# Kernel tuning notes

Hardware: AMD Instinct MI355X
Metric: run time of the kernel (lower is better)

Reference implementation:

```python
import jax, jax.numpy as jnp
import numpy as np

N_STEPS = 2
MAX_STEP = 1.0
EPS64 = float(np.finfo(np.float64).eps)


def _sphere_log(p, q):
    # log map on unit sphere, tangent at p pointing to q; p,q: [..., D]
    cos = jnp.clip(jnp.sum(p * q, axis=-1, keepdims=True), -1.0, 1.0)
    u = q - cos * p
    un = jnp.linalg.norm(u, axis=-1, keepdims=True)
    theta = jnp.arccos(cos)
    return theta * u / (un + 1e-12)


def _sphere_exp(p, v):
    # exp map on unit sphere; jnp.sinc(n/pi) = sin(n)/n (stable at 0)
    n = jnp.linalg.norm(v, axis=-1, keepdims=True)
    x = jnp.cos(n) * p + jnp.sinc(n / jnp.pi) * v
    return x / jnp.linalg.norm(x, axis=-1, keepdims=True)


def setup_inputs() -> dict:
    key = jax.random.key(0)
    ks = jax.random.split(key, 6)
    N, C, D, E = 50000, 16, 3, 1600000
    nodes = jax.random.normal(ks[0], (N, C, D), dtype=jnp.float32)
    nodes = nodes / jnp.linalg.norm(nodes, axis=-1, keepdims=True)  # points on S^2
    edge_w = jax.random.uniform(ks[1], (E,), dtype=jnp.float32)
    senders = jax.random.randint(ks[2], (E,), 0, N, dtype=jnp.int32)
    receivers = jax.random.randint(ks[3], (E,), 0, N, dtype=jnp.int32)
    t_sqrt = 1.0 + 0.3 * jax.random.normal(ks[4], (C,), dtype=jnp.float32)
    delta_sqrt = 1.0 + 0.3 * jax.random.normal(ks[5], (C,), dtype=jnp.float32)
    return {"nodes": nodes, "edge_w": edge_w, "t_sqrt": t_sqrt,
            "delta_sqrt": delta_sqrt, "senders": senders, "receivers": receivers}


def reference(nodes, edge_w, t_sqrt, delta_sqrt, senders, receivers):
    N = nodes.shape[0]
    t = (t_sqrt ** 2) / N_STEPS            # per-channel time, split across Euler steps
    delta = delta_sqrt ** 2                 # per-channel min step size
    deg = jax.ops.segment_sum(edge_w, senders, num_segments=N)  # [N]

    def laplace(x):
        # graph Laplacian of manifold-valued signal: weighted mean of log maps, negated
        logs = _sphere_log(x[senders], x[receivers])              # [E, C, D]
        agg = jax.ops.segment_sum(edge_w[:, None, None] * logs, senders, num_segments=N)
        return -agg / (deg[:, None, None] + 1e-12)                # [N, C, D]

    def step(x, _):
        v = laplace(x)
        nrm = jnp.sqrt(jnp.sum(v * v, axis=-1) + EPS64)           # [N, C]
        alp = jax.nn.sigmoid(nrm - delta[None, :])
        scale = jnp.where(nrm * alp <= MAX_STEP, alp, MAX_STEP / nrm)
        v = -(v * scale[..., None]) * t[None, :, None]
        return _sphere_exp(x, v), None

    x, _ = jax.lax.scan(step, nodes, None, length=N_STEPS, unroll=N_STEPS)
    return x
```

## Files before the change

kernel.cpp:

```cpp
#include <hip/hip_runtime.h>
#include <math.h>


constexpr float EPS64F = 2.2204460492503131e-16f;
constexpr float PI_F   = 3.14159265358979323846f;

typedef int   vi4 __attribute__((ext_vector_type(4)));
typedef float vf4 __attribute__((ext_vector_type(4)));

__global__ __launch_bounds__(256) void hist_kernel(
    const vi4* __restrict__ snd4, int* __restrict__ counts,
    vi4* __restrict__ pos4, const int* __restrict__ snd,
    int* __restrict__ pos, int E) {
  int i = blockIdx.x * 256 + threadIdx.x;
  int E4 = E >> 2;
  if (i < E4) {
    vi4 s = __builtin_nontemporal_load(&snd4[i]);
    vi4 p;
    p.x = atomicAdd(&counts[s.x], 1);
    p.y = atomicAdd(&counts[s.y], 1);
    p.z = atomicAdd(&counts[s.z], 1);
    p.w = atomicAdd(&counts[s.w], 1);
    __builtin_nontemporal_store(p, &pos4[i]);
  }
  if (i == 0) {
    for (int e = E4 << 2; e < E; ++e) pos[e] = atomicAdd(&counts[snd[e]], 1);
  }
}

__global__ __launch_bounds__(1024) void scanA_kernel(
    const int* __restrict__ counts, int* __restrict__ row_start,
    int* __restrict__ btot, int N) {
  __shared__ int wsum[16];
  int tid = threadIdx.x;
  int lane = tid & 63, wave = tid >> 6;
  int i = blockIdx.x * 1024 + tid;
  int v = (i < N) ? counts[i] : 0;
  int incl = v;
  #pragma unroll
  for (int off = 1; off < 64; off <<= 1) {
    int t = __shfl_up(incl, off, 64);
    if (lane >= off) incl += t;
  }
  if (lane == 63) wsum[wave] = incl;
  __syncthreads();
  if (wave == 0 && lane < 16) {
    int wincl = wsum[lane];
    #pragma unroll
    for (int off = 1; off < 16; off <<= 1) {
      int t = __shfl_up(wincl, off, 64);
      if (lane >= off) wincl += t;
    }
    wsum[lane] = wincl;
  }
  __syncthreads();
  int woff = (wave > 0) ? wsum[wave - 1] : 0;
  if (i < N) row_start[i] = woff + incl - v;
  if (tid == 0) btot[blockIdx.x] = wsum[15];
}

__global__ __launch_bounds__(64) void scanB_kernel(
    const int* __restrict__ btot, int* __restrict__ boff,
    int* __restrict__ row_start, int nb, int N) {
  int lane = threadIdx.x;
  int v = (lane < nb) ? btot[lane] : 0;
  int incl = v;
  #pragma unroll
  for (int off = 1; off < 64; off <<= 1) {
    int t = __shfl_up(incl, off, 64);
    if (lane >= off) incl += t;
  }
  if (lane < nb) boff[lane] = incl - v;
  if (lane == 63) row_start[N] = incl;
}

__global__ __launch_bounds__(1024) void scanC_kernel(
    int* __restrict__ row_start, const int* __restrict__ boff, int N) {
  int i = blockIdx.x * 1024 + threadIdx.x;
  if (i < N) row_start[i] += boff[blockIdx.x];
}

__global__ __launch_bounds__(256) void fill_kernel(
    const vi4* __restrict__ snd4, const vi4* __restrict__ rcv4,
    const vf4* __restrict__ ew4, const vi4* __restrict__ pos4,
    const int* __restrict__ row_start, long long* __restrict__ pair,
    const int* __restrict__ snd, const int* __restrict__ rcv,
    const float* __restrict__ ew, const int* __restrict__ pos, int E) {
  int i = blockIdx.x * 256 + threadIdx.x;
  int E4 = E >> 2;
  if (i < E4) {
    vi4 s = __builtin_nontemporal_load(&snd4[i]);
    vi4 r = __builtin_nontemporal_load(&rcv4[i]);
    vf4 w = __builtin_nontemporal_load(&ew4[i]);
    vi4 p = __builtin_nontemporal_load(&pos4[i]);
    pair[row_start[s.x] + p.x] =
        (long long)(((unsigned long long)(unsigned)__float_as_int(w.x) << 32) | (unsigned)r.x);
    pair[row_start[s.y] + p.y] =
        (long long)(((unsigned long long)(unsigned)__float_as_int(w.y) << 32) | (unsigned)r.y);
    pair[row_start[s.z] + p.z] =
        (long long)(((unsigned long long)(unsigned)__float_as_int(w.z) << 32) | (unsigned)r.z);
    pair[row_start[s.w] + p.w] =
        (long long)(((unsigned long long)(unsigned)__float_as_int(w.w) << 32) | (unsigned)r.w);
  }
  if (i == 0) {
    for (int e = E4 << 2; e < E; ++e) {
      pair[row_start[snd[e]] + pos[e]] =
          (long long)(((unsigned long long)(unsigned)__float_as_int(ew[e]) << 32) | (unsigned)rcv[e]);
    }
  }
}

__device__ __forceinline__ void edge_accum(
    float p0, float p1, float p2, float q0, float q1, float q2, float w,
    float& a0, float& a1, float& a2) {
  float cs = fminf(1.0f, fmaxf(-1.0f, fmaf(p0, q0, fmaf(p1, q1, p2 * q2))));
  float u0 = fmaf(-cs, p0, q0);
  float u1 = fmaf(-cs, p1, q1);
  float u2 = fmaf(-cs, p2, q2);
  float un2 = fmaxf(fmaf(u0, u0, fmaf(u1, u1, u2 * u2)), 1e-24f);
  float ax = fabsf(cs);
  float s = sqrtf(1.0f - ax);
  float poly = fmaf(ax, fmaf(ax, fmaf(ax, -0.0187293f, 0.0742610f),
                             -0.2121144f), 1.5707288f);
  float th = s * poly;
  float theta = (cs >= 0.0f) ? th : (PI_F - th);
  float coef = w * theta * __builtin_amdgcn_rsqf(un2);
  a0 = fmaf(coef, u0, a0);
  a1 = fmaf(coef, u1, a1);
  a2 = fmaf(coef, u2, a2);
}

__global__ __launch_bounds__(256) void flow_kernel(
    const float* __restrict__ xin, const int* __restrict__ row_start,
    const long long* __restrict__ pair, const float* __restrict__ tsq,
    const float* __restrict__ dsq, float* __restrict__ xout, int N) {
  int node = blockIdx.x * 4 + (threadIdx.x >> 6);
  if (node >= N) return;
  int lane = threadIdx.x & 63;
  int c = lane & 15;
  int k = lane >> 4;
  int beg = row_start[node];
  int end = row_start[node + 1];
  int ip = node * 48 + c * 3;
  float p0 = xin[ip + 0], p1 = xin[ip + 1], p2 = xin[ip + 2];
  float a0 = 0.f, a1 = 0.f, a2 = 0.f, ws = 0.f;
  int iters = (end - beg + 7) >> 3;
  int lastj = end - 1;
  int j = beg + k;
  for (int t = 0; t < iters; ++t, j += 8) {
    int jA = j, jB = j + 4;
    long long eA = __builtin_nontemporal_load(&pair[min(jA, lastj)]);
    long long eB = __builtin_nontemporal_load(&pair[min(jB, lastj)]);
    int rA = (int)eA;
    int rB = (int)eB;
    float wA = (jA < end) ? __int_as_float((int)(eA >> 32)) : 0.f;
    float wB = (jB < end) ? __int_as_float((int)(eB >> 32)) : 0.f;
    const float* qA = xin + rA * 48 + c * 3;
    const float* qB = xin + rB * 48 + c * 3;
    float qA0 = qA[0], qA1 = qA[1], qA2 = qA[2];
    float qB0 = qB[0], qB1 = qB[1], qB2 = qB[2];
    edge_accum(p0, p1, p2, qA0, qA1, qA2, wA, a0, a1, a2);
    edge_accum(p0, p1, p2, qB0, qB1, qB2, wB, a0, a1, a2);
    ws += wA + wB;
  }
  a0 += __shfl_xor(a0, 16); a1 += __shfl_xor(a1, 16);
  a2 += __shfl_xor(a2, 16); ws += __shfl_xor(ws, 16);
  a0 += __shfl_xor(a0, 32); a1 += __shfl_xor(a1, 32);
  a2 += __shfl_xor(a2, 32); ws += __shfl_xor(ws, 32);
  float invdg = __builtin_amdgcn_rcpf(ws + 1e-12f);
  float g0 = a0 * invdg, g1 = a1 * invdg, g2 = a2 * invdg;
  float nrm = sqrtf(fmaf(g0, g0, fmaf(g1, g1, g2 * g2)) + EPS64F);
  float ts = tsq[c];
  float tch = ts * ts * 0.5f;
  float dsv = dsq[c];
  float dch = dsv * dsv;
  float alp = __builtin_amdgcn_rcpf(1.0f + __expf(dch - nrm));
  float scale = (nrm * alp <= 1.0f) ? alp : __builtin_amdgcn_rcpf(nrm);
  float f = scale * tch;
  float v0 = g0 * f, v1 = g1 * f, v2 = g2 * f;
  float nv = sqrtf(fmaf(v0, v0, fmaf(v1, v1, v2 * v2)));
  float cn = __cosf(nv);
  float sc = (nv > 1e-20f) ? (__sinf(nv) * __builtin_amdgcn_rcpf(nv)) : 1.0f;
  float y0 = fmaf(cn, p0, sc * v0);
  float y1 = fmaf(cn, p1, sc * v1);
  float y2 = fmaf(cn, p2, sc * v2);
  float inv = __builtin_amdgcn_rsqf(fmaf(y0, y0, fmaf(y1, y1, y2 * y2)));
  if (k == 0) {
    xout[ip + 0] = y0 * inv;
    xout[ip + 1] = y1 * inv;
    xout[ip + 2] = y2 * inv;
  }
}

extern "C" void kernel_launch(void* const* d_in, const int* in_sizes, int n_in,
                              void* d_out, int out_size, void* d_ws, size_t ws_size,
                              hipStream_t stream) {
  const float* nodes = (const float*)d_in[0];
  const float* ew    = (const float*)d_in[1];
  const float* tsq   = (const float*)d_in[2];
  const float* dsq   = (const float*)d_in[3];
  const int*   snd   = (const int*)d_in[4];
  const int*   rcv   = (const int*)d_in[5];
  float* out = (float*)d_out;

  int E = in_sizes[1];
  int N = in_sizes[0] / 48;

  int*       counts    = (int*)d_ws;
  int*       row_start = counts + N;
  int*       btot      = row_start + (N + 4);
  int*       boff      = btot + 64;
  long long* pair      = (long long*)(boff + 64);
  int*       pos       = (int*)(pair + E);
  float*     xtmp      = (float*)pos;

  hipMemsetAsync(counts, 0, sizeof(int) * (size_t)N, stream);

  int E4 = E >> 2;
  int eb = (E4 + 255) / 256;
  int nb = (N + 1023) / 1024;
  int fb = (N + 3) / 4;

  hist_kernel<<<eb, 256, 0, stream>>>((const vi4*)snd, counts, (vi4*)pos,
                                      snd, pos, E);
  scanA_kernel<<<nb, 1024, 0, stream>>>(counts, row_start, btot, N);
  scanB_kernel<<<1, 64, 0, stream>>>(btot, boff, row_start, nb, N);
  scanC_kernel<<<nb, 1024, 0, stream>>>(row_start, boff, N);
  fill_kernel<<<eb, 256, 0, stream>>>((const vi4*)snd, (const vi4*)rcv,
                                      (const vf4*)ew, (const vi4*)pos,
                                      row_start, pair, snd, rcv, ew, pos, E);

  flow_kernel<<<fb, 256, 0, stream>>>(nodes, row_start, pair, tsq, dsq, xtmp, N);
  flow_kernel<<<fb, 256, 0, stream>>>(xtmp, row_start, pair, tsq, dsq, out, N);
}
```

Before: 301.6 us.

## Replicate histogram counters across 8 copies to reduce atomic contention in CSR build

The sender histogram now uses 8 replicated counter arrays, picked by block index, so concurrent atomics spread over more addresses. The scan kernel merges the replicas into per-node totals and turns each replica into an exclusive prefix within the node. scanC then adds the row start so the fill kernel can look up its slot from its own replica. This costs 8x memset and more scan traffic in exchange for less atomic serialization on the same counters.

```diff
diff --git a/kernel.cpp b/kernel.cpp
--- a/kernel.cpp
+++ b/kernel.cpp
@@ -4,38 +4,53 @@
 
 constexpr float EPS64F = 2.2204460492503131e-16f;
 constexpr float PI_F   = 3.14159265358979323846f;
+constexpr int   NREP   = 8;
 
 typedef int   vi4 __attribute__((ext_vector_type(4)));
 typedef float vf4 __attribute__((ext_vector_type(4)));
 
 __global__ __launch_bounds__(256) void hist_kernel(
-    const vi4* __restrict__ snd4, int* __restrict__ counts,
+    const vi4* __restrict__ snd4, int* __restrict__ rep,
     vi4* __restrict__ pos4, const int* __restrict__ snd,
-    int* __restrict__ pos, int E) {
+    int* __restrict__ pos, int N, int E) {
   int i = blockIdx.x * 256 + threadIdx.x;
+  int rb = (blockIdx.x & (NREP - 1)) * N;
   int E4 = E >> 2;
   if (i < E4) {
     vi4 s = __builtin_nontemporal_load(&snd4[i]);
     vi4 p;
-    p.x = atomicAdd(&counts[s.x], 1);
-    p.y = atomicAdd(&counts[s.y], 1);
-    p.z = atomicAdd(&counts[s.z], 1);
-    p.w = atomicAdd(&counts[s.w], 1);
+    p.x = atomicAdd(&rep[rb + s.x], 1);
+    p.y = atomicAdd(&rep[rb + s.y], 1);
+    p.z = atomicAdd(&rep[rb + s.z], 1);
+    p.w = atomicAdd(&rep[rb + s.w], 1);
     __builtin_nontemporal_store(p, &pos4[i]);
   }
   if (i == 0) {
-    for (int e = E4 << 2; e < E; ++e) pos[e] = atomicAdd(&counts[snd[e]], 1);
+    for (int e = E4 << 2; e < E; ++e) pos[e] = atomicAdd(&rep[snd[e]], 1);
   }
 }
 
 __global__ __launch_bounds__(1024) void scanA_kernel(
-    const int* __restrict__ counts, int* __restrict__ row_start,
+    int* __restrict__ rep, int* __restrict__ row_start,
     int* __restrict__ btot, int N) {
   __shared__ int wsum[16];
   int tid = threadIdx.x;
   int lane = tid & 63, wave = tid >> 6;
   int i = blockIdx.x * 1024 + tid;
-  int v = (i < N) ? counts[i] : 0;
+  int v = 0;
+  if (i < N) {
+    int run = 0;
+    int cpre[NREP];
+    #pragma unroll
+    for (int r = 0; r < NREP; ++r) {
+      int t = rep[r * N + i];
+      cpre[r] = run;
+      run += t;
+    }
+    v = run;
+    #pragma unroll
+    for (int r = 0; r < NREP; ++r) rep[r * N + i] = cpre[r];
+  }
   int incl = v;
   #pragma unroll
   for (int off = 1; off < 64; off <<= 1) {
@@ -75,36 +90,43 @@
 }
 
 __global__ __launch_bounds__(1024) void scanC_kernel(
-    int* __restrict__ row_start, const int* __restrict__ boff, int N) {
+    int* __restrict__ row_start, const int* __restrict__ boff,
+    int* __restrict__ rep, int N) {
   int i = blockIdx.x * 1024 + threadIdx.x;
-  if (i < N) row_start[i] += boff[blockIdx.x];
+  if (i < N) {
+    int rs = row_start[i] + boff[blockIdx.x];
+    row_start[i] = rs;
+    #pragma unroll
+    for (int r = 0; r < NREP; ++r) rep[r * N + i] += rs;
+  }
 }
 
 __global__ __launch_bounds__(256) void fill_kernel(
     const vi4* __restrict__ snd4, const vi4* __restrict__ rcv4,
     const vf4* __restrict__ ew4, const vi4* __restrict__ pos4,
-    const int* __restrict__ row_start, long long* __restrict__ pair,
+    const int* __restrict__ rep, long long* __restrict__ pair,
     const int* __restrict__ snd, const int* __restrict__ rcv,
-    const float* __restrict__ ew, const int* __restrict__ pos, int E) {
+    const float* __restrict__ ew, const int* __restrict__ pos, int N, int E) {
   int i = blockIdx.x * 256 + threadIdx.x;
+  int rb = (blockIdx.x & (NREP - 1)) * N;
   int E4 = E >> 2;
   if (i < E4) {
     vi4 s = __builtin_nontemporal_load(&snd4[i]);
     vi4 r = __builtin_nontemporal_load(&rcv4[i]);
     vf4 w = __builtin_nontemporal_load(&ew4[i]);
     vi4 p = __builtin_nontemporal_load(&pos4[i]);
-    pair[row_start[s.x] + p.x] =
+    pair[rep[rb + s.x] + p.x] =
         (long long)(((unsigned long long)(unsigned)__float_as_int(w.x) << 32) | (unsigned)r.x);
-    pair[row_start[s.y] + p.y] =
+    pair[rep[rb + s.y] + p.y] =
         (long long)(((unsigned long long)(unsigned)__float_as_int(w.y) << 32) | (unsigned)r.y);
-    pair[row_start[s.z] + p.z] =
+    pair[rep[rb + s.z] + p.z] =
         (long long)(((unsigned long long)(unsigned)__float_as_int(w.z) << 32) | (unsigned)r.z);
-    pair[row_start[s.w] + p.w] =
+    pair[rep[rb + s.w] + p.w] =
         (long long)(((unsigned long long)(unsigned)__float_as_int(w.w) << 32) | (unsigned)r.w);
   }
   if (i == 0) {
     for (int e = E4 << 2; e < E; ++e) {
-      pair[row_start[snd[e]] + pos[e]] =
+      pair[rep[snd[e]] + pos[e]] =
           (long long)(((unsigned long long)(unsigned)__float_as_int(ew[e]) << 32) | (unsigned)rcv[e]);
     }
   }
@@ -206,29 +228,29 @@
   int E = in_sizes[1];
   int N = in_sizes[0] / 48;
 
-  int*       counts    = (int*)d_ws;
-  int*       row_start = counts + N;
+  int*       rep       = (int*)d_ws;
+  int*       row_start = rep + NREP * N;
   int*       btot      = row_start + (N + 4);
   int*       boff      = btot + 64;
   long long* pair      = (long long*)(boff + 64);
   int*       pos       = (int*)(pair + E);
   float*     xtmp      = (float*)pos;
 
-  hipMemsetAsync(counts, 0, sizeof(int) * (size_t)N, stream);
+  hipMemsetAsync(rep, 0, sizeof(int) * (size_t)(NREP * N), stream);
 
   int E4 = E >> 2;
   int eb = (E4 + 255) / 256;
   int nb = (N + 1023) / 1024;
   int fb = (N + 3) / 4;
 
-  hist_kernel<<<eb, 256, 0, stream>>>((const vi4*)snd, counts, (vi4*)pos,
-                                      snd, pos, E);
-  scanA_kernel<<<nb, 1024, 0, stream>>>(counts, row_start, btot, N);
+  hist_kernel<<<eb, 256, 0, stream>>>((const vi4*)snd, rep, (vi4*)pos,
+                                      snd, pos, N, E);
+  scanA_kernel<<<nb, 1024, 0, stream>>>(rep, row_start, btot, N);
   scanB_kernel<<<1, 64, 0, stream>>>(btot, boff, row_start, nb, N);
-  scanC_kernel<<<nb, 1024, 0, stream>>>(row_start, boff, N);
+  scanC_kernel<<<nb, 1024, 0, stream>>>(row_start, boff, rep, N);
   fill_kernel<<<eb, 256, 0, stream>>>((const vi4*)snd, (const vi4*)rcv,
                                       (const vf4*)ew, (const vi4*)pos,
-                                      row_start, pair, snd, rcv, ew, pos, E);
+                                      rep, pair, snd, rcv, ew, pos, N, E);
 
   flow_kernel<<<fb, 256, 0, stream>>>(nodes, row_start, pair, tsq, dsq, xtmp, N);
   flow_kernel<<<fb, 256, 0, stream>>>(xtmp, row_start, pair, tsq, dsq, out, N);
```

Result: no change. 300.0 us (-0.5%).
